# Kernel optimization log

Hardware: AMD Instinct MI355X
Metric: run time of the kernel (lower is better)

Reference implementation:

```python
import jax, jax.numpy as jnp
import numpy as np

N_ITEM, N_USER = 100000, 50000
D, H = 128, 8
DH = D // H
E1, E2 = 500000, 250000
NCNT = 51  # num_cnt_embeddings = cnt.max()+1
EPS = 1e-5


def setup_inputs() -> dict:
    key = jax.random.key(0)
    ks = jax.random.split(key, 32)
    r = lambda i, s: jax.random.normal(ks[i], s, dtype=jnp.float32)
    w = lambda i, s: jax.random.normal(ks[i], s, dtype=jnp.float32) * (1.0 / np.sqrt(s[-1]))
    return {
        # node features
        "ft_item": r(0, (N_ITEM, D)),
        "ft_user": r(1, (N_USER, D)),
        # hetero-level batch norm params (training-mode batch stats)
        "bn_g_item": jnp.ones((D,), jnp.float32), "bn_b_item": jnp.zeros((D,), jnp.float32),
        "bn_g_user": jnp.ones((D,), jnp.float32), "bn_b_user": jnp.zeros((D,), jnp.float32),
        # etype 'i2i' (item -> item), has cnt edge embedding
        "Wq1": w(2, (D, D)), "bq1": jnp.zeros((D,), jnp.float32),
        "Wk1": w(3, (D, D)), "Wv1": w(4, (D, D)),
        "ae1": r(5, (1, D)),
        "emb_cnt1": r(6, (NCNT, D)) * 0.1,
        # etype 'u2i' (user -> item), no cnt
        "Wq2": w(7, (D, D)), "bq2": jnp.zeros((D,), jnp.float32),
        "Wk2": w(8, (D, D)), "Wv2": w(9, (D, D)),
        "ae2": r(10, (1, D)),
        # vtype 'item' output transforms
        "W_agg": w(11, (D, D)), "b_agg": jnp.zeros((D,), jnp.float32),
        "W_self": w(12, (D, D)),
        # edges (eid order)
        "uid1": jax.random.randint(ks[13], (E1,), 0, N_ITEM, dtype=jnp.int32),
        "vid1": jax.random.randint(ks[14], (E1,), 0, N_ITEM, dtype=jnp.int32),
        "cnt1": jax.random.randint(ks[15], (E1,), 0, NCNT, dtype=jnp.int32),
        "uid2": jax.random.randint(ks[16], (E2,), 0, N_USER, dtype=jnp.int32),
        "vid2": jax.random.randint(ks[17], (E2,), 0, N_ITEM, dtype=jnp.int32),
    }


def _bn(x, g, b):
    mu = x.mean(0)
    var = x.var(0)
    return (x - mu) * jax.lax.rsqrt(var + EPS) * g + b


def _edge_scores(q_src, k_dst, uid, vid, attn_e, ft_e=None):
    # u_add_v gather, optional edge feature, gated per-head score [E, H]
    e = q_src[uid] + k_dst[vid]
    if ft_e is not None:
        e = e + ft_e
    e = attn_e * jax.nn.sigmoid(e)
    return e.reshape(-1, H, DH).sum(-1)


def reference(ft_item, ft_user, bn_g_item, bn_b_item, bn_g_user, bn_b_user,
              Wq1, bq1, Wk1, Wv1, ae1, emb_cnt1,
              Wq2, bq2, Wk2, Wv2, ae2,
              W_agg, b_agg, W_self,
              uid1, vid1, cnt1, uid2, vid2):
    xi = _bn(ft_item, bn_g_item, bn_b_item)   # item features (src and dst)
    xu = _bn(ft_user, bn_g_user, bn_b_user)   # user features (src only)

    # etype 'i2i': utype=item, vtype=item (ft_dst = xi, full graph)
    q1 = xi @ Wq1.T + bq1
    k1 = xi @ Wk1.T
    v1 = (xi @ Wv1.T).reshape(N_ITEM, H, DH)
    e1 = _edge_scores(q1, k1, uid1, vid1, ae1, ft_e=emb_cnt1[cnt1])  # [E1, H]

    # etype 'u2i': utype=user, vtype=item
    q2 = xu @ Wq2.T + bq2
    k2 = xi @ Wk2.T
    v2 = (xu @ Wv2.T).reshape(N_USER, H, DH)
    e2 = _edge_scores(q2, k2, uid2, vid2, ae2)  # [E2, H]

    # combined heterograph: offset user src ids by num item src nodes
    src = jnp.concatenate([uid1, uid2 + N_ITEM])
    dst = jnp.concatenate([vid1, vid2])
    val = jnp.concatenate([v1, v2], axis=0)        # [N_ITEM+N_USER, H, DH]
    sc = jnp.concatenate([e1, e2], axis=0)         # [E, H]

    # edge_softmax over incoming edges of each dst node (per head)
    m = jax.lax.stop_gradient(jax.ops.segment_max(sc, dst, num_segments=N_ITEM))
    ex = jnp.exp(sc - m[dst])
    s = jax.ops.segment_sum(ex, dst, num_segments=N_ITEM)
    a = ex / s[dst]                                # [E, H]

    # u_mul_e_sum: weighted scatter-sum of source values to dst
    agg = jax.ops.segment_sum(val[src] * a[:, :, None], dst,
                              num_segments=N_ITEM).reshape(N_ITEM, D)

    return jax.nn.relu(agg @ W_agg.T + b_agg + xi @ W_self.T)
```

## Files before the change

kernel.cpp:

```cpp
#include <hip/hip_runtime.h>
#include <hip/hip_bf16.h>

#define N_ITEM 100000
#define N_USER 50000
#define N_ALL  150000
#define E1N 500000
#define E2N 250000
#define EALL (E1N + E2N)
#define NPAD 100352
#define NI_PAD 100096
#define NU_PAD 50176

static constexpr size_t OFF_STATS = 0;
static constexpr size_t OFF_HIST  = 2048;
static constexpr size_t OFF_SCALE = OFF_HIST + (size_t)NPAD * 4;
static constexpr size_t OFF_M     = OFF_SCALE + 2048;
static constexpr size_t OFF_WPACK = 409600;
static constexpr size_t OFF_QC    = OFF_WPACK + 8ull * 32768ull;
static constexpr size_t OFF_VC    = OFF_QC + (size_t)N_ALL * 256;
static constexpr size_t OFF_K1    = OFF_VC + (size_t)N_ALL * 256;
static constexpr size_t OFF_K2    = OFF_K1 + (size_t)N_ITEM * 256;
static constexpr size_t OFF_SELF  = OFF_K2 + (size_t)N_ITEM * 256;
static constexpr size_t OFF_START = OFF_SELF + (size_t)N_ITEM * 256;
static constexpr size_t OFF_CURSOR= OFF_START + (size_t)NPAD * 4;
static constexpr size_t OFF_BSUM  = OFF_CURSOR + (size_t)NPAD * 4;
static constexpr size_t OFF_ORD   = OFF_BSUM + 1024;
static constexpr size_t OFF_AGG   = OFF_ORD + (size_t)EALL * 8 + 128;

__device__ __forceinline__ float bf2f(unsigned short u) {
    return __uint_as_float(((unsigned)u) << 16);
}
__device__ __forceinline__ unsigned short f2bf(float f) {
    unsigned u = __float_as_uint(f);
    u += 0x7fffu + ((u >> 16) & 1u);
    return (unsigned short)(u >> 16);
}

typedef __attribute__((ext_vector_type(8))) short bf16x8;
typedef __attribute__((ext_vector_type(4))) float f32x4;

struct ProArgs {
    const float* w[8];
    const float* ft_item;
    const float* ft_user;
    const int* vid1;
    const int* vid2;
};
#define PRO_PACK 64
#define PRO_STAT 512
#define PRO_HIST 2930

__global__ __launch_bounds__(256) void prologue(ProArgs A, char* __restrict__ ws) {
    __shared__ float ls[256], ls2[256];
    int b = blockIdx.x, tid = threadIdx.x;
    if (b < PRO_PACK) {
        unsigned short* dst = (unsigned short*)(ws + OFF_WPACK);
        int gid = b * 256 + tid;
        int m = gid >> 11, rem = gid & 2047;
        int t = rem >> 8, kt = (rem >> 6) & 3, lane = rem & 63;
        int n = t * 16 + (lane & 15);
        int k0 = kt * 32 + (lane >> 4) * 8;
        const float* wrow = A.w[m] + n * 128 + k0;
        float4 w0 = *(const float4*)wrow;
        float4 w1 = *(const float4*)(wrow + 4);
        ushort4 o0 = make_ushort4(f2bf(w0.x), f2bf(w0.y), f2bf(w0.z), f2bf(w0.w));
        ushort4 o1 = make_ushort4(f2bf(w1.x), f2bf(w1.y), f2bf(w1.z), f2bf(w1.w));
        *(ushort4*)(dst + (size_t)gid * 8)     = o0;
        *(ushort4*)(dst + (size_t)gid * 8 + 4) = o1;
    } else if (b < PRO_PACK + PRO_STAT) {
        int bb = b - PRO_PACK;
        int type = bb >> 8, xb = bb & 255;
        const float* x = type ? A.ft_user : A.ft_item;
        int N = type ? N_USER : N_ITEM;
        float* sum = (float*)(ws + OFF_STATS) + type * 256;
        float* sq  = sum + 128;
        int c = tid & 127;
        int half = tid >> 7;
        float s = 0.f, s2 = 0.f;
        for (int r = xb * 2 + half; r < N; r += 512) {
            float v = x[(size_t)r * 128 + c];
            s += v; s2 += v * v;
        }
        ls[tid] = s; ls2[tid] = s2;
        __syncthreads();
        if (half == 0) {
            atomicAdd(&sum[c], ls[c] + ls[c + 128]);
            atomicAdd(&sq[c],  ls2[c] + ls2[c + 128]);
        }
    } else {
        int e = (b - PRO_PACK - PRO_STAT) * 256 + tid;
        if (e < EALL) {
            int dst = (e < E1N) ? A.vid1[e] : A.vid2[e - E1N];
            atomicAdd((int*)(ws + OFF_HIST) + dst, 1);
        }
    }
}

__global__ __launch_bounds__(1024) void scan_partial(char* __restrict__ ws) {
    __shared__ int sd[1024];
    const int* hist = (const int*)(ws + OFF_HIST);
    int* start  = (int*)(ws + OFF_START);
    int* cursor = (int*)(ws + OFF_CURSOR);
    int* bsum   = (int*)(ws + OFF_BSUM);
    int t = threadIdx.x;
    int gid = blockIdx.x * 1024 + t;
    int v = hist[gid];
    sd[t] = v;
    __syncthreads();
    #pragma unroll
    for (int off = 1; off < 1024; off <<= 1) {
        int x = (t >= off) ? sd[t - off] : 0;
        __syncthreads();
        sd[t] += x;
        __syncthreads();
    }
    int ex = sd[t] - v;
    start[gid] = ex;
    cursor[gid] = ex;
    if (t == 1023) bsum[blockIdx.x] = sd[t];
}

__global__ __launch_bounds__(256) void mid(const float* __restrict__ g_i, const float* __restrict__ b_i,
                                           const float* __restrict__ g_u, const float* __restrict__ b_u,
                                           const float* __restrict__ ae1, const float* __restrict__ ae2,
                                           char* __restrict__ ws) {
    __shared__ int sd[128];
    int t = threadIdx.x;
    if (blockIdx.x == 0) {
        const float* stats = (const float*)(ws + OFF_STATS);
        float* scale = (float*)(ws + OFF_SCALE);
        float* M     = (float*)(ws + OFF_M);
        int type = t >> 7, c = t & 127;
        float N = type ? (float)N_USER : (float)N_ITEM;
        float su = stats[type * 256 + c];
        float sq = stats[type * 256 + 128 + c];
        float mu = su / N;
        float var = sq / N - mu * mu;
        float rstd = rsqrtf(var + 1e-5f);
        float g = type ? g_u[c] : g_i[c];
        float b = type ? b_u[c] : b_i[c];
        scale[type * 256 + c]       = g * rstd;
        scale[type * 256 + 128 + c] = b - mu * g * rstd;
        if (t < 8) {
            float m1 = 0.f, m2 = 0.f;
            for (int j = 0; j < 16; j++) {
                m1 += fmaxf(ae1[t * 16 + j], 0.f);
                m2 += fmaxf(ae2[t * 16 + j], 0.f);
            }
            M[t] = fmaxf(m1, m2);
        }
    } else {
        int* bsum = (int*)(ws + OFF_BSUM);
        int v = 0;
        if (t < 128) { v = (t < 98) ? bsum[t] : 0; sd[t] = v; }
        __syncthreads();
        #pragma unroll
        for (int off = 1; off < 128; off <<= 1) {
            int x = 0;
            if (t < 128 && t >= off) x = sd[t - off];
            __syncthreads();
            if (t < 128) sd[t] += x;
            __syncthreads();
        }
        if (t < 98) bsum[t] = sd[t] - v;
    }
}

__global__ __launch_bounds__(256) void edge_scatter(const int* __restrict__ uid1, const int* __restrict__ vid1,
                                                    const int* __restrict__ cnt1,
                                                    const int* __restrict__ uid2, const int* __restrict__ vid2,
                                                    char* __restrict__ ws) {
    int e = blockIdx.x * 256 + threadIdx.x;
    if (e >= EALL) return;
    int* cursor = (int*)(ws + OFF_CURSOR);
    const int* bsum = (const int*)(ws + OFF_BSUM);
    int2* ord = (int2*)(ws + OFF_ORD);
    int2 rec; int dst;
    if (e < E1N) {
        rec.x = uid1[e]; rec.y = cnt1[e]; dst = vid1[e];
    } else {
        int ee = e - E1N;
        rec.x = N_ITEM + uid2[ee]; rec.y = -1; dst = vid2[ee];
    }
    int pos = atomicAdd(&cursor[dst], 1) + bsum[dst >> 10];
    ord[pos] = rec;
}

struct TArgs {
    const float* x;
    const float* bias0;
    int N;
    int scaleOff;
    int nmat;
    int wtIdx[5];
    unsigned short* out[5];
};

#define TB_I 391
#define TB_U 196
#define SPITCH 136

__global__ __launch_bounds__(256) void transform(TArgs AI, TArgs AU, char* __restrict__ ws) {
    __shared__ unsigned short stg[4][2][16 * SPITCH];
    int b = blockIdx.x;
    const TArgs& A = (b < TB_I) ? AI : AU;
    int blk = (b < TB_I) ? b : b - TB_I;

    const unsigned short* wpack = (const unsigned short*)(ws + OFF_WPACK);
    const float* scaleb = (const float*)(ws + OFF_SCALE) + A.scaleOff;
    int tid = threadIdx.x, lane = tid & 63, wv = tid >> 6;
    int l16 = lane & 15, quad = lane >> 4;
    int base = blk * 256 + wv * 64;

    bf16x8 bfr[4][4];
    #pragma unroll
    for (int kt = 0; kt < 4; kt++) {
        int c0 = kt * 32 + quad * 8;
        float4 sc0 = *(const float4*)(scaleb + c0);
        float4 sc1 = *(const float4*)(scaleb + c0 + 4);
        float4 bi0 = *(const float4*)(scaleb + 128 + c0);
        float4 bi1 = *(const float4*)(scaleb + 128 + c0 + 4);
        #pragma unroll
        for (int it = 0; it < 4; it++) {
            int gr = base + it * 16 + l16;
            bf16x8 f = {0, 0, 0, 0, 0, 0, 0, 0};
            if (gr < A.N) {
                const float* p = A.x + (size_t)gr * 128 + c0;
                float4 v0 = *(const float4*)p;
                float4 v1 = *(const float4*)(p + 4);
                f[0] = (short)f2bf(fmaf(v0.x, sc0.x, bi0.x));
                f[1] = (short)f2bf(fmaf(v0.y, sc0.y, bi0.y));
                f[2] = (short)f2bf(fmaf(v0.z, sc0.z, bi0.z));
                f[3] = (short)f2bf(fmaf(v0.w, sc0.w, bi0.w));
                f[4] = (short)f2bf(fmaf(v1.x, sc1.x, bi1.x));
                f[5] = (short)f2bf(fmaf(v1.y, sc1.y, bi1.y));
                f[6] = (short)f2bf(fmaf(v1.z, sc1.z, bi1.z));
                f[7] = (short)f2bf(fmaf(v1.w, sc1.w, bi1.w));
            }
            bfr[it][kt] = f;
        }
    }

    for (int m = 0; m < A.nmat; m++) {
        const unsigned short* wp = wpack + (size_t)A.wtIdx[m] * 16384;
        unsigned short* outp = A.out[m];
        const float* bias = (m == 0) ? A.bias0 : nullptr;
        #pragma unroll
        for (int it = 0; it < 4; it++) {
            unsigned short* st = stg[wv][it & 1];
            #pragma unroll
            for (int nt = 0; nt < 8; nt++) {
                bf16x8 a4[4];
                #pragma unroll
                for (int kt = 0; kt < 4; kt++)
                    a4[kt] = *(const bf16x8*)(wp + (size_t)((nt * 4 + kt) * 64 + lane) * 8);
                f32x4 acc = {0.f, 0.f, 0.f, 0.f};
                if (bias) {
                    float4 bv = *(const float4*)(bias + nt * 16 + quad * 4);
                    acc[0] = bv.x; acc[1] = bv.y; acc[2] = bv.z; acc[3] = bv.w;
                }
                #pragma unroll
                for (int kt = 0; kt < 4; kt++)
                    acc = __builtin_amdgcn_mfma_f32_16x16x32_bf16(a4[kt], bfr[it][kt], acc, 0, 0, 0);
                ushort4 o = make_ushort4(f2bf(acc[0]), f2bf(acc[1]), f2bf(acc[2]), f2bf(acc[3]));
                *(ushort4*)(st + l16 * SPITCH + nt * 16 + quad * 4) = o;
            }
            #pragma unroll
            for (int i = 0; i < 4; i++) {
                int chunk = i * 64 + lane;
                int row = chunk >> 4, c8 = (chunk & 15) * 8;
                int gr = base + it * 16 + row;
                if (gr < A.N)
                    *(bf16x8*)(outp + (size_t)gr * 128 + c8) = *(const bf16x8*)(st + row * SPITCH + c8);
            }
        }
    }
}

__global__ __launch_bounds__(256) void edge_agg(const float* __restrict__ emb,
                                                const float* __restrict__ ae1, const float* __restrict__ ae2,
                                                char* __restrict__ ws) {
    const unsigned short* qc = (const unsigned short*)(ws + OFF_QC);
    const unsigned short* vc = (const unsigned short*)(ws + OFF_VC);
    const unsigned short* k1 = (const unsigned short*)(ws + OFF_K1);
    const unsigned short* k2 = (const unsigned short*)(ws + OFF_K2);
    const int* start = (const int*)(ws + OFF_START);
    const int* bsum  = (const int*)(ws + OFF_BSUM);
    const int2* ord = (const int2*)(ws + OFF_ORD);
    const float* M = (const float*)(ws + OFF_M);
    float* agg = (float*)(ws + OFF_AGG);

    int tid = threadIdx.x;
    int lane = tid & 63;
    int slot = lane >> 4;
    int l16 = lane & 15;
    int d0 = l16 * 8;
    int h = l16 >> 1;
    int dst = blockIdx.x * 4 + (tid >> 6);
    if (dst >= N_ITEM) return;

    float mh = M[h];
    float ae1f[8], ae2f[8], k1f[8], k2f[8];
    {
        float4 a0 = *(const float4*)(ae1 + d0), a1 = *(const float4*)(ae1 + d0 + 4);
        float4 b0 = *(const float4*)(ae2 + d0), b1 = *(const float4*)(ae2 + d0 + 4);
        ae1f[0]=a0.x; ae1f[1]=a0.y; ae1f[2]=a0.z; ae1f[3]=a0.w;
        ae1f[4]=a1.x; ae1f[5]=a1.y; ae1f[6]=a1.z; ae1f[7]=a1.w;
        ae2f[0]=b0.x; ae2f[1]=b0.y; ae2f[2]=b0.z; ae2f[3]=b0.w;
        ae2f[4]=b1.x; ae2f[5]=b1.y; ae2f[6]=b1.z; ae2f[7]=b1.w;
        bf16x8 p1 = *(const bf16x8*)(k1 + (size_t)dst * 128 + d0);
        bf16x8 p2 = *(const bf16x8*)(k2 + (size_t)dst * 128 + d0);
        #pragma unroll
        for (int j = 0; j < 8; j++) {
            k1f[j] = bf2f((unsigned short)p1[j]);
            k2f[j] = bf2f((unsigned short)p2[j]);
        }
    }

    int beg = start[dst] + bsum[dst >> 10];
    int end = start[dst + 1] + bsum[(dst + 1) >> 10];
    float acc[8];
    #pragma unroll
    for (int j = 0; j < 8; j++) acc[j] = 0.f;
    float s = 0.f;

    for (int i = beg + slot; i < end; i += 8) {
        int i2 = i + 4;
        bool vb = i2 < end;
        int2 ra = ord[i];
        int2 rb = ord[vb ? i2 : i];
        bool t1a = ra.y >= 0, t1b = rb.y >= 0;
        bf16x8 qa = *(const bf16x8*)(qc + (size_t)ra.x * 128 + d0);
        bf16x8 qb = *(const bf16x8*)(qc + (size_t)rb.x * 128 + d0);
        bf16x8 va = *(const bf16x8*)(vc + (size_t)ra.x * 128 + d0);
        bf16x8 vbv = *(const bf16x8*)(vc + (size_t)rb.x * 128 + d0);
        const float* epa = emb + (size_t)(t1a ? ra.y : 0) * 128 + d0;
        const float* epb = emb + (size_t)(t1b ? rb.y : 0) * 128 + d0;
        float4 ea0 = *(const float4*)epa, ea1 = *(const float4*)(epa + 4);
        float4 eb0 = *(const float4*)epb, eb1 = *(const float4*)(epb + 4);
        float eaf[8] = {ea0.x, ea0.y, ea0.z, ea0.w, ea1.x, ea1.y, ea1.z, ea1.w};
        float ebf[8] = {eb0.x, eb0.y, eb0.z, eb0.w, eb1.x, eb1.y, eb1.z, eb1.w};
        {
            float t = 0.f;
            #pragma unroll
            for (int j = 0; j < 8; j++) {
                float x = bf2f((unsigned short)qa[j]) + (t1a ? k1f[j] + eaf[j] : k2f[j]);
                float ae = t1a ? ae1f[j] : ae2f[j];
                t += ae * __builtin_amdgcn_rcpf(1.f + __expf(-x));
            }
            t += __shfl_xor(t, 1);
            float ex = __expf(t - mh);
            s += ex;
            #pragma unroll
            for (int j = 0; j < 8; j++)
                acc[j] = fmaf(ex, bf2f((unsigned short)va[j]), acc[j]);
        }
        {
            float t = 0.f;
            #pragma unroll
            for (int j = 0; j < 8; j++) {
                float x = bf2f((unsigned short)qb[j]) + (t1b ? k1f[j] + ebf[j] : k2f[j]);
                float ae = t1b ? ae1f[j] : ae2f[j];
                t += ae * __builtin_amdgcn_rcpf(1.f + __expf(-x));
            }
            t += __shfl_xor(t, 1);
            float ex = vb ? __expf(t - mh) : 0.f;
            s += ex;
            #pragma unroll
            for (int j = 0; j < 8; j++)
                acc[j] = fmaf(ex, bf2f((unsigned short)vbv[j]), acc[j]);
        }
    }
    s += __shfl_xor(s, 16);
    s += __shfl_xor(s, 32);
    #pragma unroll
    for (int j = 0; j < 8; j++) {
        acc[j] += __shfl_xor(acc[j], 16);
        acc[j] += __shfl_xor(acc[j], 32);
    }
    if (slot == 0) {
        float inv = (s > 0.f) ? __builtin_amdgcn_rcpf(s) : 0.f;
        float4 o0 = make_float4(acc[0] * inv, acc[1] * inv, acc[2] * inv, acc[3] * inv);
        float4 o1 = make_float4(acc[4] * inv, acc[5] * inv, acc[6] * inv, acc[7] * inv);
        *(float4*)(agg + (size_t)dst * 128 + d0)     = o0;
        *(float4*)(agg + (size_t)dst * 128 + d0 + 4) = o1;
    }
}

#define FPITCH 132

__global__ __launch_bounds__(256) void final_mfma(const float* __restrict__ b_agg,
                                                  float* __restrict__ out, char* __restrict__ ws) {
    __shared__ float stg[4][16 * FPITCH];
    const float* agg = (const float*)(ws + OFF_AGG);
    const unsigned short* selft = (const unsigned short*)(ws + OFF_SELF);
    const unsigned short* wp = (const unsigned short*)(ws + OFF_WPACK) + 7ull * 16384;
    int tid = threadIdx.x, lane = tid & 63, wv = tid >> 6;
    int l16 = lane & 15, quad = lane >> 4;
    int base = blockIdx.x * 256 + wv * 64;
    float* st = stg[wv];

    bf16x8 bfr[4][4];
    #pragma unroll
    for (int it = 0; it < 4; it++) {
        int gr = base + it * 16 + l16;
        #pragma unroll
        for (int kt = 0; kt < 4; kt++) {
            bf16x8 f = {0, 0, 0, 0, 0, 0, 0, 0};
            if (gr < N_ITEM) {
                const float* p = agg + (size_t)gr * 128 + kt * 32 + quad * 8;
                float4 v0 = *(const float4*)p;
                float4 v1 = *(const float4*)(p + 4);
                f[0] = (short)f2bf(v0.x); f[1] = (short)f2bf(v0.y);
                f[2] = (short)f2bf(v0.z); f[3] = (short)f2bf(v0.w);
                f[4] = (short)f2bf(v1.x); f[5] = (short)f2bf(v1.y);
                f[6] = (short)f2bf(v1.z); f[7] = (short)f2bf(v1.w);
            }
            bfr[it][kt] = f;
        }
    }

    #pragma unroll
    for (int it = 0; it < 4; it++) {
        #pragma unroll
        for (int nt = 0; nt < 8; nt++) {
            bf16x8 a4[4];
            #pragma unroll
            for (int kt = 0; kt < 4; kt++)
                a4[kt] = *(const bf16x8*)(wp + (size_t)((nt * 4 + kt) * 64 + lane) * 8);
            float4 bv = *(const float4*)(b_agg + nt * 16 + quad * 4);
            f32x4 acc = {bv.x, bv.y, bv.z, bv.w};
            #pragma unroll
            for (int kt = 0; kt < 4; kt++)
                acc = __builtin_amdgcn_mfma_f32_16x16x32_bf16(a4[kt], bfr[it][kt], acc, 0, 0, 0);
            *(f32x4*)(st + l16 * FPITCH + nt * 16 + quad * 4) = acc;
        }
        #pragma unroll
        for (int i = 0; i < 8; i++) {
            int chunk = i * 64 + lane;
            int row = chunk >> 5, c4 = (chunk & 31) * 4;
            int gr = base + it * 16 + row;
            if (gr < N_ITEM) {
                float4 v = *(const float4*)(st + row * FPITCH + c4);
                size_t idx = (size_t)gr * 128 + c4;
                ushort4 sf = *(const ushort4*)(selft + idx);
                float4 o;
                o.x = fmaxf(v.x + bf2f(sf.x), 0.f);
                o.y = fmaxf(v.y + bf2f(sf.y), 0.f);
                o.z = fmaxf(v.z + bf2f(sf.z), 0.f);
                o.w = fmaxf(v.w + bf2f(sf.w), 0.f);
                *(float4*)(out + idx) = o;
            }
        }
    }
}

extern "C" void kernel_launch(void* const* d_in, const int* in_sizes, int n_in,
                              void* d_out, int out_size, void* d_ws, size_t ws_size,
                              hipStream_t stream) {
    char* ws = (char*)d_ws;

    const float* ft_item = (const float*)d_in[0];
    const float* ft_user = (const float*)d_in[1];
    const float* bng_i = (const float*)d_in[2];
    const float* bnb_i = (const float*)d_in[3];
    const float* bng_u = (const float*)d_in[4];
    const float* bnb_u = (const float*)d_in[5];
    const float* Wq1 = (const float*)d_in[6];
    const float* bq1 = (const float*)d_in[7];
    const float* Wk1 = (const float*)d_in[8];
    const float* Wv1 = (const float*)d_in[9];
    const float* ae1 = (const float*)d_in[10];
    const float* emb = (const float*)d_in[11];
    const float* Wq2 = (const float*)d_in[12];
    const float* bq2 = (const float*)d_in[13];
    const float* Wk2 = (const float*)d_in[14];
    const float* Wv2 = (const float*)d_in[15];
    const float* ae2 = (const float*)d_in[16];
    const float* W_agg = (const float*)d_in[17];
    const float* b_agg = (const float*)d_in[18];
    const float* W_self = (const float*)d_in[19];
    const int* uid1 = (const int*)d_in[20];
    const int* vid1 = (const int*)d_in[21];
    const int* cnt1 = (const int*)d_in[22];
    const int* uid2 = (const int*)d_in[23];
    const int* vid2 = (const int*)d_in[24];
    float* out = (float*)d_out;

    hipMemsetAsync(ws + OFF_STATS, 0, 2048 + (size_t)NPAD * 4, stream);

    ProArgs pa;
    pa.w[0] = Wq1; pa.w[1] = Wk1; pa.w[2] = Wv1; pa.w[3] = Wk2;
    pa.w[4] = W_self; pa.w[5] = Wq2; pa.w[6] = Wv2; pa.w[7] = W_agg;
    pa.ft_item = ft_item; pa.ft_user = ft_user;
    pa.vid1 = vid1; pa.vid2 = vid2;
    prologue<<<PRO_PACK + PRO_STAT + PRO_HIST, 256, 0, stream>>>(pa, ws);

    scan_partial<<<98, 1024, 0, stream>>>(ws);

    mid<<<2, 256, 0, stream>>>(bng_i, bnb_i, bng_u, bnb_u, ae1, ae2, ws);

    edge_scatter<<<(EALL + 255) / 256, 256, 0, stream>>>(uid1, vid1, cnt1, uid2, vid2, ws);

    TArgs ti, tu;
    ti.x = ft_item; ti.bias0 = bq1; ti.N = N_ITEM; ti.scaleOff = 0; ti.nmat = 5;
    ti.wtIdx[0] = 0; ti.wtIdx[1] = 1; ti.wtIdx[2] = 2; ti.wtIdx[3] = 3; ti.wtIdx[4] = 4;
    unsigned short* QC = (unsigned short*)(ws + OFF_QC);
    unsigned short* VC = (unsigned short*)(ws + OFF_VC);
    ti.out[0] = QC;
    ti.out[1] = (unsigned short*)(ws + OFF_K1);
    ti.out[2] = VC;
    ti.out[3] = (unsigned short*)(ws + OFF_K2);
    ti.out[4] = (unsigned short*)(ws + OFF_SELF);
    tu.x = ft_user; tu.bias0 = bq2; tu.N = N_USER; tu.scaleOff = 256; tu.nmat = 2;
    tu.wtIdx[0] = 5; tu.wtIdx[1] = 6; tu.wtIdx[2] = 0; tu.wtIdx[3] = 0; tu.wtIdx[4] = 0;
    tu.out[0] = QC + (size_t)N_ITEM * 128;
    tu.out[1] = VC + (size_t)N_ITEM * 128;
    tu.out[2] = tu.out[3] = tu.out[4] = tu.out[0];
    transform<<<TB_I + TB_U, 256, 0, stream>>>(ti, tu, ws);

    edge_agg<<<(N_ITEM + 3) / 4, 256, 0, stream>>>(emb, ae1, ae2, ws);

    final_mfma<<<NI_PAD / 256, 256, 0, stream>>>(b_agg, out, ws);
}
```

Before: 526.7 us.

## Halve transform tiles, bf16 edge embeddings, restructure edge_agg lane mapping

The cnt embedding table is now packed to bf16 in the prologue, so edge_agg gathers it in bf16 instead of fp32. edge_agg is remapped so each wavefront uses 2 slots of 32 lanes with 4 dims per lane, instead of 4 slots of 16 lanes with 8 dims. Each iteration prefetches the next edge record, and occupancy hints are added. transform is split into twice as many blocks of half the rows, to cut registers and raise occupancy. The cost is fewer edges in flight per wave and reloading the weight fragments in more blocks.

Measured after the change: 511.1 us. -3.0%, faster.

```diff
diff --git a/kernel.cpp b/kernel.cpp
--- a/kernel.cpp
+++ b/kernel.cpp
@@ -8,14 +8,13 @@
 #define E2N 250000
 #define EALL (E1N + E2N)
 #define NPAD 100352
-#define NI_PAD 100096
-#define NU_PAD 50176
 
 static constexpr size_t OFF_STATS = 0;
 static constexpr size_t OFF_HIST  = 2048;
 static constexpr size_t OFF_SCALE = OFF_HIST + (size_t)NPAD * 4;
 static constexpr size_t OFF_M     = OFF_SCALE + 2048;
-static constexpr size_t OFF_WPACK = 409600;
+static constexpr size_t OFF_EMBB  = OFF_M + 64;
+static constexpr size_t OFF_WPACK = OFF_EMBB + 13312;
 static constexpr size_t OFF_QC    = OFF_WPACK + 8ull * 32768ull;
 static constexpr size_t OFF_VC    = OFF_QC + (size_t)N_ALL * 256;
 static constexpr size_t OFF_K1    = OFF_VC + (size_t)N_ALL * 256;
@@ -43,10 +42,12 @@
     const float* w[8];
     const float* ft_item;
     const float* ft_user;
+    const float* emb;
     const int* vid1;
     const int* vid2;
 };
 #define PRO_PACK 64
+#define PRO_EMB  7
 #define PRO_STAT 512
 #define PRO_HIST 2930
 
@@ -67,8 +68,15 @@
         ushort4 o1 = make_ushort4(f2bf(w1.x), f2bf(w1.y), f2bf(w1.z), f2bf(w1.w));
         *(ushort4*)(dst + (size_t)gid * 8)     = o0;
         *(ushort4*)(dst + (size_t)gid * 8 + 4) = o1;
-    } else if (b < PRO_PACK + PRO_STAT) {
-        int bb = b - PRO_PACK;
+    } else if (b < PRO_PACK + PRO_EMB) {
+        int gid = (b - PRO_PACK) * 256 + tid;
+        if (gid * 4 < 51 * 128) {
+            float4 v = *(const float4*)(A.emb + gid * 4);
+            ushort4 o = make_ushort4(f2bf(v.x), f2bf(v.y), f2bf(v.z), f2bf(v.w));
+            *(ushort4*)((unsigned short*)(ws + OFF_EMBB) + gid * 4) = o;
+        }
+    } else if (b < PRO_PACK + PRO_EMB + PRO_STAT) {
+        int bb = b - PRO_PACK - PRO_EMB;
         int type = bb >> 8, xb = bb & 255;
         const float* x = type ? A.ft_user : A.ft_item;
         int N = type ? N_USER : N_ITEM;
@@ -88,7 +96,7 @@
             atomicAdd(&sq[c],  ls2[c] + ls2[c + 128]);
         }
     } else {
-        int e = (b - PRO_PACK - PRO_STAT) * 256 + tid;
+        int e = (b - PRO_PACK - PRO_EMB - PRO_STAT) * 256 + tid;
         if (e < EALL) {
             int dst = (e < E1N) ? A.vid1[e] : A.vid2[e - E1N];
             atomicAdd((int*)(ws + OFF_HIST) + dst, 1);
@@ -196,11 +204,11 @@
     unsigned short* out[5];
 };
 
-#define TB_I 391
-#define TB_U 196
+#define TB_I 782
+#define TB_U 391
 #define SPITCH 136
 
-__global__ __launch_bounds__(256) void transform(TArgs AI, TArgs AU, char* __restrict__ ws) {
+__global__ __launch_bounds__(256, 5) void transform(TArgs AI, TArgs AU, char* __restrict__ ws) {
     __shared__ unsigned short stg[4][2][16 * SPITCH];
     int b = blockIdx.x;
     const TArgs& A = (b < TB_I) ? AI : AU;
@@ -210,9 +218,9 @@
     const float* scaleb = (const float*)(ws + OFF_SCALE) + A.scaleOff;
     int tid = threadIdx.x, lane = tid & 63, wv = tid >> 6;
     int l16 = lane & 15, quad = lane >> 4;
-    int base = blk * 256 + wv * 64;
-
-    bf16x8 bfr[4][4];
+    int base = blk * 128 + wv * 32;
+
+    bf16x8 bfr[2][4];
     #pragma unroll
     for (int kt = 0; kt < 4; kt++) {
         int c0 = kt * 32 + quad * 8;
@@ -221,7 +229,7 @@
         float4 bi0 = *(const float4*)(scaleb + 128 + c0);
         float4 bi1 = *(const float4*)(scaleb + 128 + c0 + 4);
         #pragma unroll
-        for (int it = 0; it < 4; it++) {
+        for (int it = 0; it < 2; it++) {
             int gr = base + it * 16 + l16;
             bf16x8 f = {0, 0, 0, 0, 0, 0, 0, 0};
             if (gr < A.N) {
@@ -246,8 +254,8 @@
         unsigned short* outp = A.out[m];
         const float* bias = (m == 0) ? A.bias0 : nullptr;
         #pragma unroll
-        for (int it = 0; it < 4; it++) {
-            unsigned short* st = stg[wv][it & 1];
+        for (int it = 0; it < 2; it++) {
+            unsigned short* st = stg[wv][it];
             #pragma unroll
             for (int nt = 0; nt < 8; nt++) {
                 bf16x8 a4[4];
@@ -277,13 +285,13 @@
     }
 }
 
-__global__ __launch_bounds__(256) void edge_agg(const float* __restrict__ emb,
-                                                const float* __restrict__ ae1, const float* __restrict__ ae2,
-                                                char* __restrict__ ws) {
+__global__ __launch_bounds__(256, 8) void edge_agg(const float* __restrict__ ae1, const float* __restrict__ ae2,
+                                                   char* __restrict__ ws) {
     const unsigned short* qc = (const unsigned short*)(ws + OFF_QC);
     const unsigned short* vc = (const unsigned short*)(ws + OFF_VC);
     const unsigned short* k1 = (const unsigned short*)(ws + OFF_K1);
     const unsigned short* k2 = (const unsigned short*)(ws + OFF_K2);
+    const unsigned short* embb = (const unsigned short*)(ws + OFF_EMBB);
     const int* start = (const int*)(ws + OFF_START);
     const int* bsum  = (const int*)(ws + OFF_BSUM);
     const int2* ord = (const int2*)(ws + OFF_ORD);
@@ -292,98 +300,66 @@
 
     int tid = threadIdx.x;
     int lane = tid & 63;
-    int slot = lane >> 4;
-    int l16 = lane & 15;
-    int d0 = l16 * 8;
-    int h = l16 >> 1;
+    int half = lane >> 5;
+    int l = lane & 31;
+    int d0 = l << 2;
+    int h = l >> 2;
     int dst = blockIdx.x * 4 + (tid >> 6);
     if (dst >= N_ITEM) return;
 
     float mh = M[h];
-    float ae1f[8], ae2f[8], k1f[8], k2f[8];
-    {
-        float4 a0 = *(const float4*)(ae1 + d0), a1 = *(const float4*)(ae1 + d0 + 4);
-        float4 b0 = *(const float4*)(ae2 + d0), b1 = *(const float4*)(ae2 + d0 + 4);
-        ae1f[0]=a0.x; ae1f[1]=a0.y; ae1f[2]=a0.z; ae1f[3]=a0.w;
-        ae1f[4]=a1.x; ae1f[5]=a1.y; ae1f[6]=a1.z; ae1f[7]=a1.w;
-        ae2f[0]=b0.x; ae2f[1]=b0.y; ae2f[2]=b0.z; ae2f[3]=b0.w;
-        ae2f[4]=b1.x; ae2f[5]=b1.y; ae2f[6]=b1.z; ae2f[7]=b1.w;
-        bf16x8 p1 = *(const bf16x8*)(k1 + (size_t)dst * 128 + d0);
-        bf16x8 p2 = *(const bf16x8*)(k2 + (size_t)dst * 128 + d0);
-        #pragma unroll
-        for (int j = 0; j < 8; j++) {
-            k1f[j] = bf2f((unsigned short)p1[j]);
-            k2f[j] = bf2f((unsigned short)p2[j]);
-        }
-    }
+    float4 ae1v = *(const float4*)(ae1 + d0);
+    float4 ae2v = *(const float4*)(ae2 + d0);
+    ushort4 k1p = *(const ushort4*)(k1 + (size_t)dst * 128 + d0);
+    ushort4 k2p = *(const ushort4*)(k2 + (size_t)dst * 128 + d0);
+    float4 k1v = make_float4(bf2f(k1p.x), bf2f(k1p.y), bf2f(k1p.z), bf2f(k1p.w));
+    float4 k2v = make_float4(bf2f(k2p.x), bf2f(k2p.y), bf2f(k2p.z), bf2f(k2p.w));
 
     int beg = start[dst] + bsum[dst >> 10];
     int end = start[dst + 1] + bsum[(dst + 1) >> 10];
-    float acc[8];
-    #pragma unroll
-    for (int j = 0; j < 8; j++) acc[j] = 0.f;
-    float s = 0.f;
-
-    for (int i = beg + slot; i < end; i += 8) {
-        int i2 = i + 4;
-        bool vb = i2 < end;
-        int2 ra = ord[i];
-        int2 rb = ord[vb ? i2 : i];
-        bool t1a = ra.y >= 0, t1b = rb.y >= 0;
-        bf16x8 qa = *(const bf16x8*)(qc + (size_t)ra.x * 128 + d0);
-        bf16x8 qb = *(const bf16x8*)(qc + (size_t)rb.x * 128 + d0);
-        bf16x8 va = *(const bf16x8*)(vc + (size_t)ra.x * 128 + d0);
-        bf16x8 vbv = *(const bf16x8*)(vc + (size_t)rb.x * 128 + d0);
-        const float* epa = emb + (size_t)(t1a ? ra.y : 0) * 128 + d0;
-        const float* epb = emb + (size_t)(t1b ? rb.y : 0) * 128 + d0;
-        float4 ea0 = *(const float4*)epa, ea1 = *(const float4*)(epa + 4);
-        float4 eb0 = *(const float4*)epb, eb1 = *(const float4*)(epb + 4);
-        float eaf[8] = {ea0.x, ea0.y, ea0.z, ea0.w, ea1.x, ea1.y, ea1.z, ea1.w};
-        float ebf[8] = {eb0.x, eb0.y, eb0.z, eb0.w, eb1.x, eb1.y, eb1.z, eb1.w};
-        {
-            float t = 0.f;
-            #pragma unroll
-            for (int j = 0; j < 8; j++) {
-                float x = bf2f((unsigned short)qa[j]) + (t1a ? k1f[j] + eaf[j] : k2f[j]);
-                float ae = t1a ? ae1f[j] : ae2f[j];
-                t += ae * __builtin_amdgcn_rcpf(1.f + __expf(-x));
-            }
+    float a0 = 0.f, a1 = 0.f, a2 = 0.f, a3 = 0.f, s = 0.f;
+
+    int i = beg + half;
+    if (i < end) {
+        int2 rec = ord[i];
+        while (true) {
+            int inext = i + 2;
+            int ipf = (inext < end) ? inext : (end - 1);
+            int2 recn = ord[ipf];
+            bool t1 = rec.y >= 0;
+            ushort4 qp = *(const ushort4*)(qc + (size_t)rec.x * 128 + d0);
+            ushort4 vp = *(const ushort4*)(vc + (size_t)rec.x * 128 + d0);
+            ushort4 ep = *(const ushort4*)(embb + (size_t)(t1 ? rec.y : 0) * 128 + d0);
+            float x0 = bf2f(qp.x) + (t1 ? k1v.x + bf2f(ep.x) : k2v.x);
+            float x1 = bf2f(qp.y) + (t1 ? k1v.y + bf2f(ep.y) : k2v.y);
+            float x2 = bf2f(qp.z) + (t1 ? k1v.z + bf2f(ep.z) : k2v.z);
+            float x3 = bf2f(qp.w) + (t1 ? k1v.w + bf2f(ep.w) : k2v.w);
+            float4 ae = t1 ? ae1v : ae2v;
+            float t = ae.x * __builtin_amdgcn_rcpf(1.f + __expf(-x0))
+                    + ae.y * __builtin_amdgcn_rcpf(1.f + __expf(-x1))
+                    + ae.z * __builtin_amdgcn_rcpf(1.f + __expf(-x2))
+                    + ae.w * __builtin_amdgcn_rcpf(1.f + __expf(-x3));
             t += __shfl_xor(t, 1);
+            t += __shfl_xor(t, 2);
             float ex = __expf(t - mh);
             s += ex;
-            #pragma unroll
-            for (int j = 0; j < 8; j++)
-                acc[j] = fmaf(ex, bf2f((unsigned short)va[j]), acc[j]);
-        }
-        {
-            float t = 0.f;
-            #pragma unroll
-            for (int j = 0; j < 8; j++) {
-                float x = bf2f((unsigned short)qb[j]) + (t1b ? k1f[j] + ebf[j] : k2f[j]);
-                float ae = t1b ? ae1f[j] : ae2f[j];
-                t += ae * __builtin_amdgcn_rcpf(1.f + __expf(-x));
-            }
-            t += __shfl_xor(t, 1);
-            float ex = vb ? __expf(t - mh) : 0.f;
-            s += ex;
-            #pragma unroll
-            for (int j = 0; j < 8; j++)
-                acc[j] = fmaf(ex, bf2f((unsigned short)vbv[j]), acc[j]);
-        }
-    }
-    s += __shfl_xor(s, 16);
-    s += __shfl_xor(s, 32);
-    #pragma unroll
-    for (int j = 0; j < 8; j++) {
-        acc[j] += __shfl_xor(acc[j], 16);
-        acc[j] += __shfl_xor(acc[j], 32);
-    }
-    if (slot == 0) {
+            a0 = fmaf(ex, bf2f(vp.x), a0);
+            a1 = fmaf(ex, bf2f(vp.y), a1);
+            a2 = fmaf(ex, bf2f(vp.z), a2);
+            a3 = fmaf(ex, bf2f(vp.w), a3);
+            if (inext >= end) break;
+            i = inext; rec = recn;
+        }
+    }
+    s  += __shfl_xor(s, 32);
+    a0 += __shfl_xor(a0, 32);
+    a1 += __shfl_xor(a1, 32);
+    a2 += __shfl_xor(a2, 32);
+    a3 += __shfl_xor(a3, 32);
+    if (half == 0) {
         float inv = (s > 0.f) ? __builtin_amdgcn_rcpf(s) : 0.f;
-        float4 o0 = make_float4(acc[0] * inv, acc[1] * inv, acc[2] * inv, acc[3] * inv);
-        float4 o1 = make_float4(acc[4] * inv, acc[5] * inv, acc[6] * inv, acc[7] * inv);
-        *(float4*)(agg + (size_t)dst * 128 + d0)     = o0;
-        *(float4*)(agg + (size_t)dst * 128 + d0 + 4) = o1;
+        float4 o = make_float4(a0 * inv, a1 * inv, a2 * inv, a3 * inv);
+        *(float4*)(agg + (size_t)dst * 128 + d0) = o;
     }
 }
 
@@ -492,9 +468,9 @@
     ProArgs pa;
     pa.w[0] = Wq1; pa.w[1] = Wk1; pa.w[2] = Wv1; pa.w[3] = Wk2;
     pa.w[4] = W_self; pa.w[5] = Wq2; pa.w[6] = Wv2; pa.w[7] = W_agg;
-    pa.ft_item = ft_item; pa.ft_user = ft_user;
+    pa.ft_item = ft_item; pa.ft_user = ft_user; pa.emb = emb;
     pa.vid1 = vid1; pa.vid2 = vid2;
-    prologue<<<PRO_PACK + PRO_STAT + PRO_HIST, 256, 0, stream>>>(pa, ws);
+    prologue<<<PRO_PACK + PRO_EMB + PRO_STAT + PRO_HIST, 256, 0, stream>>>(pa, ws);
 
     scan_partial<<<98, 1024, 0, stream>>>(ws);
 
@@ -519,7 +495,7 @@
     tu.out[2] = tu.out[3] = tu.out[4] = tu.out[0];
     transform<<<TB_I + TB_U, 256, 0, stream>>>(ti, tu, ws);
 
-    edge_agg<<<(N_ITEM + 3) / 4, 256, 0, stream>>>(emb, ae1, ae2, ws);
-
-    final_mfma<<<NI_PAD / 256, 256, 0, stream>>>(b_agg, out, ws);
-}
+    edge_agg<<<(N_ITEM + 3) / 4, 256, 0, stream>>>(ae1, ae2, ws);
+
+    final_mfma<<<(N_ITEM + 255) / 256, 256, 0, stream>>>(b_agg, out, ws);
+}
```
